# Kernel optimization log

Hardware: AMD Instinct MI355X
Metric: run time of the kernel (lower is better)

## Reference

```python
import jax, jax.numpy as jnp
import numpy as np

N_EMBD = 768
HEAD_SIZE = 64
B, T = 32, 1024


def setup_inputs() -> dict:
    key = jax.random.key(0)
    k1, k2, k3, k4 = jax.random.split(key, 4)
    x = jax.random.normal(k1, (B, T, N_EMBD), dtype=jnp.float32)
    Wq = jax.random.normal(k2, (N_EMBD, HEAD_SIZE), dtype=jnp.float32) * 0.02
    Wk = jax.random.normal(k3, (N_EMBD, HEAD_SIZE), dtype=jnp.float32) * 0.02
    Wv = jax.random.normal(k4, (N_EMBD, HEAD_SIZE), dtype=jnp.float32) * 0.02
    return {"x": x, "Wq": Wq, "Wk": Wk, "Wv": Wv}


def _apply_rope(q, k):
    # q, k: [B, T, D]; interleaved (even/odd) RoPE exactly as the torch source
    seq_len, dim = q.shape[-2], q.shape[-1]
    pos = jnp.arange(seq_len, dtype=jnp.float32)[:, None]                      # [T, 1]
    div_term = jnp.exp(jnp.arange(0, dim, 2, dtype=jnp.float32) * (-jnp.log(10000.0) / dim))  # [D/2]
    sin_emb = jnp.sin(pos * div_term)                                          # [T, D/2]
    cos_emb = jnp.cos(pos * div_term)                                          # [T, D/2]

    def rot(t):
        te, to = t[..., ::2], t[..., 1::2]
        re = te * cos_emb - to * sin_emb
        ro = te * sin_emb + to * cos_emb
        # interleave back: [..., T, D/2, 2] -> [..., T, D]
        return jnp.stack([re, ro], axis=-1).reshape(t.shape)

    return rot(q), rot(k)


def reference(x, Wq, Wk, Wv):
    Bx, Tx, C = x.shape  # C == n_embd
    q = x @ Wq  # [B, T, D]
    k = x @ Wk
    v = x @ Wv
    q, k = _apply_rope(q, k)
    # NOTE: source scales by C**-0.5 where C = n_embd, not head_size
    wei = jnp.einsum('btd,bsd->bts', q, k) * (C ** -0.5)  # [B, T, T]
    causal = jnp.tril(jnp.ones((Tx, Tx), dtype=bool))
    wei = jnp.where(causal, wei, -jnp.inf)
    wei = jax.nn.softmax(wei, axis=-1)
    # dropout is identity in eval mode
    out = jnp.einsum('bts,bsd->btd', wei, v)  # [B, T, D]
    return out
```

## Files before the change

### kernel.cpp

```cpp
#include <hip/hip_runtime.h>
#include <cmath>

#define B 32
#define T 1024
#define CDIM 768
#define D 64
#define SCALE 0.03608439182435161f
#define XSTR 72

typedef short bf16x8 __attribute__((ext_vector_type(8)));
typedef float f32x4 __attribute__((ext_vector_type(4)));
typedef unsigned short u16x8 __attribute__((ext_vector_type(8)));

__device__ inline ushort f2bf(float f) {
  union { float f; unsigned u; } v{f};
  unsigned r = (v.u + 0x7FFFu + ((v.u >> 16) & 1u)) >> 16;
  return (ushort)r;
}

__global__ __launch_bounds__(256) void wt_prep(
    const float* __restrict__ Wq, const float* __restrict__ Wk,
    const float* __restrict__ Wv, ushort* __restrict__ Wt)
{
  const int n   = blockIdx.x;
  const int sel = n >> 6, col = n & 63;
  const float* W = (sel == 0) ? Wq : (sel == 1) ? Wk : Wv;
  const float sc = (sel == 0) ? SCALE : 1.f;
  for (int k = threadIdx.x; k < CDIM; k += 256)
    Wt[(size_t)n * CDIM + k] = f2bf(W[(size_t)k * D + col] * sc);
}

__global__ __launch_bounds__(256) void proj_mfma(
    const float* __restrict__ x,
    const ushort* __restrict__ Wt,
    ushort* __restrict__ qkv)
{
  const int t    = threadIdx.x;
  const int lane = t & 63;
  const int wid  = t >> 6;
  const int ln16 = lane & 15;
  const int quad = lane >> 4;
  const int row0 = blockIdx.x * 64;

  __shared__ ushort Xs[2][64 * XSTR];
  __shared__ ushort Ws[2][192 * XSTR];

  f32x4 acc[12];
  #pragma unroll
  for (int nt = 0; nt < 12; ++nt) acc[nt] = (f32x4){0.f, 0.f, 0.f, 0.f};

  float4 xp[2][4];
  u16x8  wp[2][6];

  auto load_stage = [&](int s, int set) {
    const int k0 = s * 64;
    #pragma unroll
    for (int it = 0; it < 4; ++it) {
      int slot = it * 256 + t, row = slot >> 4, kq = slot & 15;
      xp[set][it] = *(const float4*)(x + (size_t)(row0 + row) * CDIM + k0 + kq * 4);
    }
    #pragma unroll
    for (int it = 0; it < 6; ++it) {
      int slot = it * 256 + t, n = slot >> 3, kb = slot & 7;
      wp[set][it] = *(const u16x8*)(Wt + (size_t)n * CDIM + k0 + kb * 8);
    }
  };

  load_stage(0, 0);
  load_stage(1, 1);
  int buf = 0;
  for (int s = 0; s < CDIM / 64; ++s) {
    const int set = s & 1;
    #pragma unroll
    for (int it = 0; it < 4; ++it) {
      int slot = it * 256 + t, row = slot >> 4, kq = slot & 15;
      ushort4 bv;
      bv.x = f2bf(xp[set][it].x); bv.y = f2bf(xp[set][it].y);
      bv.z = f2bf(xp[set][it].z); bv.w = f2bf(xp[set][it].w);
      *(ushort4*)&Xs[buf][row * XSTR + kq * 4] = bv;
    }
    #pragma unroll
    for (int it = 0; it < 6; ++it) {
      int slot = it * 256 + t, n = slot >> 3, kb = slot & 7;
      *(u16x8*)&Ws[buf][n * XSTR + kb * 8] = wp[set][it];
    }
    __syncthreads();
    if (s + 2 < CDIM / 64) load_stage(s + 2, set);

    #pragma unroll
    for (int ks = 0; ks < 2; ++ks) {
      bf16x8 a = *(const bf16x8*)&Xs[buf][(wid * 16 + ln16) * XSTR + ks * 32 + quad * 8];
      #pragma unroll
      for (int nt = 0; nt < 12; ++nt) {
        bf16x8 bb = *(const bf16x8*)&Ws[buf][(nt * 16 + ln16) * XSTR + ks * 32 + quad * 8];
        acc[nt] = __builtin_amdgcn_mfma_f32_16x16x32_bf16(a, bb, acc[nt], 0, 0, 0);
      }
    }
    buf ^= 1;
  }

  #pragma unroll
  for (int nt = 0; nt < 12; ++nt) {
    const int sel = nt >> 2;
    const int d   = (nt & 3) * 16 + ln16;
    ushort* outb = qkv + (size_t)sel * (B * T * D);
    if (sel < 2) {
      const float freq = __expf((float)(d & 62) * (-0.14391156855801f));
      const float sgn  = (d & 1) ? 1.f : -1.f;
      #pragma unroll
      for (int reg = 0; reg < 4; ++reg) {
        int rowg = row0 + wid * 16 + quad * 4 + reg;
        float s, c;
        __sincosf((float)(rowg & (T - 1)) * freq, &s, &c);
        float val = acc[nt][reg];
        float partner = __shfl_xor(val, 1, 64);
        outb[(size_t)rowg * D + d] = f2bf(fmaf(sgn * partner, s, val * c));
      }
    } else {
      #pragma unroll
      for (int reg = 0; reg < 4; ++reg) {
        int rowg = row0 + wid * 16 + quad * 4 + reg;
        outb[(size_t)rowg * D + d] = f2bf(acc[nt][reg]);
      }
    }
  }
}

__global__ __launch_bounds__(256) void attn_mfma(
    const ushort* __restrict__ qg,
    const ushort* __restrict__ kg,
    const ushort* __restrict__ vg,
    float* __restrict__ out)
{
  const int t    = threadIdx.x;
  const int lane = t & 63;
  const int wid  = t >> 6;
  const int ln16 = lane & 15;
  const int quad = lane >> 4;
  const int qt   = 15 - (int)blockIdx.x;
  const int b    = blockIdx.y;

  __shared__ ushort Ks[2][64 * XSTR];
  __shared__ ushort Vt[2][64 * XSTR];
  __shared__ ushort Pl[64 * XSTR];

  bf16x8 qf[2];
  {
    const ushort* qrow = qg + (size_t)(b * T + qt * 64 + wid * 16 + ln16) * D;
    qf[0] = *(const bf16x8*)(qrow + quad * 8);
    qf[1] = *(const bf16x8*)(qrow + quad * 8 + 32);
  }

  f32x4 O[4];
  #pragma unroll
  for (int nt = 0; nt < 4; ++nt) O[nt] = (f32x4){0.f, 0.f, 0.f, 0.f};
  float mo = -1e30f, l = 0.f;

  const int kb = t & 15, db = t >> 4;
  const int d0 = db * 4, kk0 = kb * 4;

  u16x8  kp[2];
  ushort4 vp[4];
  auto load_kv = [&](int kt) {
    #pragma unroll
    for (int i = 0; i < 2; ++i) {
      int slot = i * 256 + t, row = slot >> 3, dblk = slot & 7;
      kp[i] = *(const u16x8*)(kg + (size_t)(b * T + kt * 64 + row) * D + dblk * 8);
    }
    #pragma unroll
    for (int i = 0; i < 4; ++i)
      vp[i] = *(const ushort4*)(vg + (size_t)(b * T + kt * 64 + kk0 + i) * D + d0);
  };

  load_kv(0);
  int buf = 0;
  for (int kt = 0; kt <= qt; ++kt) {
    #pragma unroll
    for (int i = 0; i < 2; ++i) {
      int slot = i * 256 + t, row = slot >> 3, dblk = slot & 7;
      *(u16x8*)&Ks[buf][row * XSTR + dblk * 8] = kp[i];
    }
    const ushort* vpe = (const ushort*)vp;
    #pragma unroll
    for (int j = 0; j < 4; ++j) {
      ushort4 c;
      c.x = vpe[0 * 4 + j]; c.y = vpe[1 * 4 + j];
      c.z = vpe[2 * 4 + j]; c.w = vpe[3 * 4 + j];
      *(ushort4*)&Vt[buf][(d0 + j) * XSTR + kk0] = c;
    }
    __syncthreads();
    if (kt < qt) load_kv(kt + 1);

    f32x4 s[4];
    #pragma unroll
    for (int mt = 0; mt < 4; ++mt) s[mt] = (f32x4){0.f, 0.f, 0.f, 0.f};
    #pragma unroll
    for (int ks = 0; ks < 2; ++ks)
      #pragma unroll
      for (int mt = 0; mt < 4; ++mt) {
        bf16x8 kf = *(const bf16x8*)&Ks[buf][(mt * 16 + ln16) * XSTR + quad * 8 + ks * 32];
        s[mt] = __builtin_amdgcn_mfma_f32_16x16x32_bf16(kf, qf[ks], s[mt], 0, 0, 0);
      }

    if (kt == qt) {
      const int ql = wid * 16 + ln16;
      #pragma unroll
      for (int mt = 0; mt < 4; ++mt)
        #pragma unroll
        for (int reg = 0; reg < 4; ++reg)
          if (mt * 16 + quad * 4 + reg > ql) s[mt][reg] = -1e30f;
    }

    float tmax = -1e30f;
    #pragma unroll
    for (int mt = 0; mt < 4; ++mt)
      #pragma unroll
      for (int reg = 0; reg < 4; ++reg) tmax = fmaxf(tmax, s[mt][reg]);
    tmax = fmaxf(tmax, __shfl_xor(tmax, 16, 64));
    tmax = fmaxf(tmax, __shfl_xor(tmax, 32, 64));
    float mn = fmaxf(mo, tmax);
    float alpha = __expf(mo - mn);
    float psum = 0.f;
    #pragma unroll
    for (int mt = 0; mt < 4; ++mt) {
      float p0 = __expf(s[mt][0] - mn), p1 = __expf(s[mt][1] - mn);
      float p2 = __expf(s[mt][2] - mn), p3 = __expf(s[mt][3] - mn);
      psum += (p0 + p1) + (p2 + p3);
      ushort4 pk;
      pk.x = f2bf(p0); pk.y = f2bf(p1); pk.z = f2bf(p2); pk.w = f2bf(p3);
      *(ushort4*)&Pl[(wid * 16 + ln16) * XSTR + mt * 16 + quad * 4] = pk;
    }
    psum += __shfl_xor(psum, 16, 64);
    psum += __shfl_xor(psum, 32, 64);
    l = alpha * l + psum;
    mo = mn;

    #pragma unroll
    for (int reg = 0; reg < 4; ++reg) {
      float av = __shfl(alpha, quad * 4 + reg, 64);
      #pragma unroll
      for (int nt = 0; nt < 4; ++nt) O[nt][reg] *= av;
    }

    bf16x8 pa[2];
    pa[0] = *(const bf16x8*)&Pl[(wid * 16 + ln16) * XSTR + quad * 8];
    pa[1] = *(const bf16x8*)&Pl[(wid * 16 + ln16) * XSTR + quad * 8 + 32];
    #pragma unroll
    for (int ks = 0; ks < 2; ++ks)
      #pragma unroll
      for (int nt = 0; nt < 4; ++nt) {
        bf16x8 vf = *(const bf16x8*)&Vt[buf][(nt * 16 + ln16) * XSTR + quad * 8 + ks * 32];
        O[nt] = __builtin_amdgcn_mfma_f32_16x16x32_bf16(pa[ks], vf, O[nt], 0, 0, 0);
      }
    buf ^= 1;
  }

  float inv = 1.f / l;
  #pragma unroll
  for (int reg = 0; reg < 4; ++reg) {
    float iv = __shfl(inv, quad * 4 + reg, 64);
    size_t row = (size_t)(b * T + qt * 64 + wid * 16 + quad * 4 + reg) * D;
    #pragma unroll
    for (int nt = 0; nt < 4; ++nt)
      out[row + nt * 16 + ln16] = O[nt][reg] * iv;
  }
}

extern "C" void kernel_launch(void* const* d_in, const int* in_sizes, int n_in,
                              void* d_out, int out_size, void* d_ws, size_t ws_size,
                              hipStream_t stream) {
  const float* x  = (const float*)d_in[0];
  const float* Wq = (const float*)d_in[1];
  const float* Wk = (const float*)d_in[2];
  const float* Wv = (const float*)d_in[3];
  float* outp = (float*)d_out;

  ushort* qkv = (ushort*)d_ws;
  ushort* Wt  = qkv + (size_t)3 * B * T * D;

  wt_prep<<<dim3(192), dim3(256), 0, stream>>>(Wq, Wk, Wv, Wt);
  proj_mfma<<<dim3((B * T) / 64), dim3(256), 0, stream>>>(x, Wt, qkv);
  attn_mfma<<<dim3(T / 64, B), dim3(256), 0, stream>>>(
      qkv, qkv + (size_t)B * T * D, qkv + 2 * (size_t)B * T * D, outp);
}
```

Baseline: 187.4 us.

## Load projection MFMA operands directly from global memory, bypassing LDS

```diff
diff --git a/kernel.cpp b/kernel.cpp
--- a/kernel.cpp
+++ b/kernel.cpp
@@ -1,4 +1,5 @@
 #include <hip/hip_runtime.h>
+#include <hip/hip_bf16.h>
 #include <cmath>
 
 #define B 32
@@ -16,6 +17,11 @@
   union { float f; unsigned u; } v{f};
   unsigned r = (v.u + 0x7FFFu + ((v.u >> 16) & 1u)) >> 16;
   return (ushort)r;
+}
+
+__device__ inline ushort2 pk2(float a, float b) {
+  __hip_bfloat162 h = __float22bfloat162_rn(float2{a, b});
+  return *(ushort2*)&h;
 }
 
 __global__ __launch_bounds__(256) void wt_prep(
@@ -30,7 +36,7 @@
     Wt[(size_t)n * CDIM + k] = f2bf(W[(size_t)k * D + col] * sc);
 }
 
-__global__ __launch_bounds__(256) void proj_mfma(
+__global__ __launch_bounds__(256, 2) void proj_mfma(
     const float* __restrict__ x,
     const ushort* __restrict__ Wt,
     ushort* __restrict__ qkv)
@@ -41,62 +47,68 @@
   const int ln16 = lane & 15;
   const int quad = lane >> 4;
   const int row0 = blockIdx.x * 64;
-
-  __shared__ ushort Xs[2][64 * XSTR];
-  __shared__ ushort Ws[2][192 * XSTR];
+  const int myrow = row0 + wid * 16 + ln16;
+
+  const float* xr = x + (size_t)myrow * CDIM + quad * 8;
+  const ushort* wp[12];
+  #pragma unroll
+  for (int nt = 0; nt < 12; ++nt)
+    wp[nt] = Wt + (size_t)(nt * 16 + ln16) * CDIM + quad * 8;
 
   f32x4 acc[12];
   #pragma unroll
   for (int nt = 0; nt < 12; ++nt) acc[nt] = (f32x4){0.f, 0.f, 0.f, 0.f};
 
   float4 xp[2][4];
-  u16x8  wp[2][6];
-
-  auto load_stage = [&](int s, int set) {
-    const int k0 = s * 64;
-    #pragma unroll
-    for (int it = 0; it < 4; ++it) {
-      int slot = it * 256 + t, row = slot >> 4, kq = slot & 15;
-      xp[set][it] = *(const float4*)(x + (size_t)(row0 + row) * CDIM + k0 + kq * 4);
-    }
-    #pragma unroll
-    for (int it = 0; it < 6; ++it) {
-      int slot = it * 256 + t, n = slot >> 3, kb = slot & 7;
-      wp[set][it] = *(const u16x8*)(Wt + (size_t)n * CDIM + k0 + kb * 8);
-    }
-  };
-
-  load_stage(0, 0);
-  load_stage(1, 1);
-  int buf = 0;
+  bf16x8 Wa[12], Wb[12];
+
+  #pragma unroll
+  for (int i = 0; i < 2; ++i) {
+    xp[0][2 * i + 0] = *(const float4*)(xr + 0 * 64 + i * 32);
+    xp[1][2 * i + 0] = *(const float4*)(xr + 1 * 64 + i * 32);
+    xp[0][2 * i + 1] = *(const float4*)(xr + 0 * 64 + i * 32 + 4);
+    xp[1][2 * i + 1] = *(const float4*)(xr + 1 * 64 + i * 32 + 4);
+  }
+  #pragma unroll
+  for (int nt = 0; nt < 12; ++nt)
+    Wa[nt] = *(const bf16x8*)(wp[nt]);
+
+  #pragma unroll
   for (int s = 0; s < CDIM / 64; ++s) {
     const int set = s & 1;
-    #pragma unroll
-    for (int it = 0; it < 4; ++it) {
-      int slot = it * 256 + t, row = slot >> 4, kq = slot & 15;
-      ushort4 bv;
-      bv.x = f2bf(xp[set][it].x); bv.y = f2bf(xp[set][it].y);
-      bv.z = f2bf(xp[set][it].z); bv.w = f2bf(xp[set][it].w);
-      *(ushort4*)&Xs[buf][row * XSTR + kq * 4] = bv;
-    }
-    #pragma unroll
-    for (int it = 0; it < 6; ++it) {
-      int slot = it * 256 + t, n = slot >> 3, kb = slot & 7;
-      *(u16x8*)&Ws[buf][n * XSTR + kb * 8] = wp[set][it];
-    }
-    __syncthreads();
-    if (s + 2 < CDIM / 64) load_stage(s + 2, set);
-
-    #pragma unroll
-    for (int ks = 0; ks < 2; ++ks) {
-      bf16x8 a = *(const bf16x8*)&Xs[buf][(wid * 16 + ln16) * XSTR + ks * 32 + quad * 8];
-      #pragma unroll
-      for (int nt = 0; nt < 12; ++nt) {
-        bf16x8 bb = *(const bf16x8*)&Ws[buf][(nt * 16 + ln16) * XSTR + ks * 32 + quad * 8];
-        acc[nt] = __builtin_amdgcn_mfma_f32_16x16x32_bf16(a, bb, acc[nt], 0, 0, 0);
-      }
-    }
-    buf ^= 1;
+    union { bf16x8 v; ushort2 u[4]; } a0, a1;
+    a0.u[0] = pk2(xp[set][0].x, xp[set][0].y);
+    a0.u[1] = pk2(xp[set][0].z, xp[set][0].w);
+    a0.u[2] = pk2(xp[set][1].x, xp[set][1].y);
+    a0.u[3] = pk2(xp[set][1].z, xp[set][1].w);
+    a1.u[0] = pk2(xp[set][2].x, xp[set][2].y);
+    a1.u[1] = pk2(xp[set][2].z, xp[set][2].w);
+    a1.u[2] = pk2(xp[set][3].x, xp[set][3].y);
+    a1.u[3] = pk2(xp[set][3].z, xp[set][3].w);
+
+    if (s + 2 < CDIM / 64) {
+      #pragma unroll
+      for (int i = 0; i < 2; ++i) {
+        xp[set][2 * i + 0] = *(const float4*)(xr + (s + 2) * 64 + i * 32);
+        xp[set][2 * i + 1] = *(const float4*)(xr + (s + 2) * 64 + i * 32 + 4);
+      }
+    }
+    #pragma unroll
+    for (int nt = 0; nt < 12; ++nt)
+      Wb[nt] = *(const bf16x8*)(wp[nt] + s * 64 + 32);
+
+    #pragma unroll
+    for (int nt = 0; nt < 12; ++nt)
+      acc[nt] = __builtin_amdgcn_mfma_f32_16x16x32_bf16(a0.v, Wa[nt], acc[nt], 0, 0, 0);
+
+    if (s + 1 < CDIM / 64) {
+      #pragma unroll
+      for (int nt = 0; nt < 12; ++nt)
+        Wa[nt] = *(const bf16x8*)(wp[nt] + (s + 1) * 64);
+    }
+    #pragma unroll
+    for (int nt = 0; nt < 12; ++nt)
+      acc[nt] = __builtin_amdgcn_mfma_f32_16x16x32_bf16(a1.v, Wb[nt], acc[nt], 0, 0, 0);
   }
 
   #pragma unroll
```

Result: slower. 242.2 us (+29.2%).
